# Kernel optimization log

Hardware: AMD Instinct MI355X
Metric: run time of the kernel (lower is better)

Reference implementation:

```python
import jax, jax.numpy as jnp
import numpy as np

FRAME = 1024
ENC = 256
HID = 128
EPS = 1e-7


def _lstm_cell(x, h, c, Wih, Whh, bih, bhh):
    # PyTorch LSTM gate order: i, f, g, o
    z = Wih @ x + bih + Whh @ h + bhh  # [4H]
    i, f, g, o = jnp.split(z, 4)
    i = jax.nn.sigmoid(i)
    f = jax.nn.sigmoid(f)
    g = jnp.tanh(g)
    o = jax.nn.sigmoid(o)
    c_new = f * c + i * g
    h_new = o * jnp.tanh(c_new)
    return h_new, c_new


def setup_inputs() -> dict:
    key = jax.random.key(0)
    ks = jax.random.split(key, 20)
    s = 0.05
    return {
        "y1": jax.random.normal(ks[0], (FRAME,), jnp.float32),
        "h1_in": jax.random.normal(ks[1], (HID,), jnp.float32),
        "c1_in": jax.random.normal(ks[2], (HID,), jnp.float32),
        "h2_in": jax.random.normal(ks[3], (HID,), jnp.float32),
        "c2_in": jax.random.normal(ks[4], (HID,), jnp.float32),
        "enc_W": jax.random.normal(ks[5], (ENC, FRAME), jnp.float32) * s,
        "gamma": jnp.ones((ENC,), jnp.float32),
        "beta": jnp.zeros((ENC,), jnp.float32),
        "Wih1": jax.random.normal(ks[6], (4 * HID, ENC), jnp.float32) * s,
        "Whh1": jax.random.normal(ks[7], (4 * HID, HID), jnp.float32) * s,
        "bih1": jax.random.normal(ks[8], (4 * HID,), jnp.float32) * s,
        "bhh1": jax.random.normal(ks[9], (4 * HID,), jnp.float32) * s,
        "Wih2": jax.random.normal(ks[10], (4 * HID, HID), jnp.float32) * s,
        "Whh2": jax.random.normal(ks[11], (4 * HID, HID), jnp.float32) * s,
        "bih2": jax.random.normal(ks[12], (4 * HID,), jnp.float32) * s,
        "bhh2": jax.random.normal(ks[13], (4 * HID,), jnp.float32) * s,
        "dense_W": jax.random.normal(ks[14], (ENC, HID), jnp.float32) * s,
        "dense_b": jax.random.normal(ks[15], (ENC,), jnp.float32) * s,
        "dec_W": jax.random.normal(ks[16], (FRAME, ENC), jnp.float32) * s,
    }


def reference(y1, h1_in, c1_in, h2_in, c2_in, enc_W, gamma, beta,
              Wih1, Whh1, bih1, bhh1, Wih2, Whh2, bih2, bhh2,
              dense_W, dense_b, dec_W):
    # encoder 1x1 conv == matvec: [256,1024] @ [1024]
    enc = enc_W @ y1  # [256]
    # global-statistic instant layer norm (mean/var over ALL elements)
    mean = jnp.mean(enc)
    sub = enc - mean
    var = jnp.mean(jnp.square(sub))
    enc_norm = (sub / jnp.sqrt(var + EPS)) * gamma + beta
    # two stateful LSTM cells (seq_len=1; dropout is identity at inference)
    h1, c1 = _lstm_cell(enc_norm, h1_in, c1_in, Wih1, Whh1, bih1, bhh1)
    h2, c2 = _lstm_cell(h1, h2_in, c2_in, Wih2, Whh2, bih2, bhh2)
    # dense + sigmoid mask on UN-normalized encoded features
    mask = jax.nn.sigmoid(dense_W @ h2 + dense_b)  # [256]
    estimated = mask * enc
    # decoder 1x1 conv == matvec: [1024,256] @ [256]
    decoded = dec_W @ estimated  # [1024]
    return (decoded.reshape(1, FRAME, 1),
            h1.reshape(1, 1, HID), c1.reshape(1, 1, HID),
            h2.reshape(1, 1, HID), c2.reshape(1, 1, HID))
```

## Files before the change

kernel.cpp:

```cpp
#include <hip/hip_runtime.h>
#include <math.h>


#define FRAME 1024
#define ENC 256
#define HID 128

__device__ __forceinline__ float sigmoidf_(float x) { return 1.0f / (1.0f + __expf(-x)); }
__device__ __forceinline__ float tanhf_(float x) { return 2.0f * sigmoidf_(2.0f * x) - 1.0f; }

__device__ __forceinline__ float wred(float v) {
#pragma unroll
    for (int o = 32; o > 0; o >>= 1) v += __shfl_xor(v, o);
    return v;
}

__global__ __launch_bounds__(256) void k_enc(const float* __restrict__ enc_W,
                                             const float* __restrict__ y1,
                                             float* __restrict__ enc_g) {
    const int t = threadIdx.x, lane = t & 63, w = t >> 6, row = blockIdx.x;
    const float4 a = reinterpret_cast<const float4*>(enc_W + row * FRAME)[t];
    const float4 b = reinterpret_cast<const float4*>(y1)[t];
    float p = a.x * b.x + a.y * b.y + a.z * b.z + a.w * b.w;
    p = wred(p);
    __shared__ float red[4];
    if (lane == 0) red[w] = p;
    __syncthreads();
    if (t == 0) enc_g[row] = red[0] + red[1] + red[2] + red[3];
}

__global__ __launch_bounds__(256) void k_z1(
    const float* __restrict__ enc_g, const float* __restrict__ gamma,
    const float* __restrict__ beta, const float* __restrict__ Wih1,
    const float* __restrict__ Whh1, const float* __restrict__ bih1,
    const float* __restrict__ bhh1, const float* __restrict__ h1_in,
    const float* __restrict__ c1_in, float* __restrict__ h1_g,
    float* __restrict__ out) {
    const int t = threadIdx.x, lane = t & 63, w = t >> 6, b = blockIdx.x;
    __shared__ __align__(16) float encN[ENC];
    __shared__ __align__(16) float hs[HID];
    __shared__ float red[8];
    __shared__ float zsh[4];

    const int r = b + HID * w;
    const float4 wa = reinterpret_cast<const float4*>(Wih1 + r * ENC)[lane];
    const float2 wb = reinterpret_cast<const float2*>(Whh1 + r * HID)[lane];
    const float bias = bih1[r] + bhh1[r];

    const float e = enc_g[t];
    const float s1 = wred(e);
    const float s2 = wred(e * e);
    if (lane == 0) { red[w] = s1; red[4 + w] = s2; }
    if (t < HID) hs[t] = h1_in[t];
    __syncthreads();
    const float mean = (red[0] + red[1] + red[2] + red[3]) * (1.f / ENC);
    const float var  = (red[4] + red[5] + red[6] + red[7]) * (1.f / ENC) - mean * mean;
    const float inv  = rsqrtf(var + 1e-7f);
    encN[t] = (e - mean) * inv * gamma[t] + beta[t];
    __syncthreads();

    const float4 xa = reinterpret_cast<const float4*>(encN)[lane];
    const float2 xb = reinterpret_cast<const float2*>(hs)[lane];
    float p = wa.x * xa.x + wa.y * xa.y + wa.z * xa.z + wa.w * xa.w
            + wb.x * xb.x + wb.y * xb.y;
    p = wred(p);
    if (lane == 0) zsh[w] = p + bias;
    __syncthreads();
    if (t == 0) {
        const float i = sigmoidf_(zsh[0]);
        const float f = sigmoidf_(zsh[1]);
        const float g = tanhf_(zsh[2]);
        const float o = sigmoidf_(zsh[3]);
        const float c = f * c1_in[b] + i * g;
        const float h = o * tanhf_(c);
        h1_g[b] = h;
        out[FRAME + b] = h;
        out[FRAME + HID + b] = c;
    }
}

__global__ __launch_bounds__(256) void k_z2(
    const float* __restrict__ h1_g, const float* __restrict__ h2_in,
    const float* __restrict__ Wih2, const float* __restrict__ Whh2,
    const float* __restrict__ bih2, const float* __restrict__ bhh2,
    const float* __restrict__ c2_in, float* __restrict__ h2_g,
    float* __restrict__ out) {
    const int t = threadIdx.x, lane = t & 63, w = t >> 6, b = blockIdx.x;
    __shared__ __align__(16) float hA[HID];
    __shared__ __align__(16) float hB[HID];
    __shared__ float zsh[4];

    const int r = b + HID * w;
    const float2 wa = reinterpret_cast<const float2*>(Wih2 + r * HID)[lane];
    const float2 wb = reinterpret_cast<const float2*>(Whh2 + r * HID)[lane];
    const float bias = bih2[r] + bhh2[r];

    if (t < HID) { hA[t] = h1_g[t]; hB[t] = h2_in[t]; }
    __syncthreads();
    const float2 xa = reinterpret_cast<const float2*>(hA)[lane];
    const float2 xb = reinterpret_cast<const float2*>(hB)[lane];
    float p = wa.x * xa.x + wa.y * xa.y + wb.x * xb.x + wb.y * xb.y;
    p = wred(p);
    if (lane == 0) zsh[w] = p + bias;
    __syncthreads();
    if (t == 0) {
        const float i = sigmoidf_(zsh[0]);
        const float f = sigmoidf_(zsh[1]);
        const float g = tanhf_(zsh[2]);
        const float o = sigmoidf_(zsh[3]);
        const float c = f * c2_in[b] + i * g;
        const float h = o * tanhf_(c);
        h2_g[b] = h;
        out[FRAME + 2 * HID + b] = h;
        out[FRAME + 3 * HID + b] = c;
    }
}

__global__ __launch_bounds__(256) void k_mask(
    const float* __restrict__ h2_g, const float* __restrict__ dense_W,
    const float* __restrict__ dense_b, const float* __restrict__ enc_g,
    float* __restrict__ est_g) {
    const int t = threadIdx.x, lane = t & 63, w = t >> 6;
    __shared__ __align__(16) float hs[HID];
    const int r = blockIdx.x * 4 + w;
    const float2 wd = reinterpret_cast<const float2*>(dense_W + r * HID)[lane];
    if (t < HID) hs[t] = h2_g[t];
    __syncthreads();
    const float2 xd = reinterpret_cast<const float2*>(hs)[lane];
    float p = wd.x * xd.x + wd.y * xd.y;
    p = wred(p);
    if (lane == 0) est_g[r] = sigmoidf_(p + dense_b[r]) * enc_g[r];
}

__global__ __launch_bounds__(256) void k_dec(
    const float* __restrict__ dec_W, const float* __restrict__ est_g,
    float* __restrict__ out) {
    const int t = threadIdx.x, lane = t & 63, w = t >> 6;
    __shared__ __align__(16) float es[ENC];
    es[t] = est_g[t];
    __syncthreads();
    const int r = blockIdx.x * 4 + w;
    const float4 a = reinterpret_cast<const float4*>(dec_W + r * ENC)[lane];
    const float4 b = reinterpret_cast<const float4*>(es)[lane];
    float p = a.x * b.x + a.y * b.y + a.z * b.z + a.w * b.w;
    p = wred(p);
    if (lane == 0) out[r] = p;
}

extern "C" void kernel_launch(void* const* d_in, const int* in_sizes, int n_in,
                              void* d_out, int out_size, void* d_ws, size_t ws_size,
                              hipStream_t stream) {
    const float* y1      = (const float*)d_in[0];
    const float* h1_in   = (const float*)d_in[1];
    const float* c1_in   = (const float*)d_in[2];
    const float* h2_in   = (const float*)d_in[3];
    const float* c2_in   = (const float*)d_in[4];
    const float* enc_W   = (const float*)d_in[5];
    const float* gamma   = (const float*)d_in[6];
    const float* beta    = (const float*)d_in[7];
    const float* Wih1    = (const float*)d_in[8];
    const float* Whh1    = (const float*)d_in[9];
    const float* bih1    = (const float*)d_in[10];
    const float* bhh1    = (const float*)d_in[11];
    const float* Wih2    = (const float*)d_in[12];
    const float* Whh2    = (const float*)d_in[13];
    const float* bih2    = (const float*)d_in[14];
    const float* bhh2    = (const float*)d_in[15];
    const float* dense_W = (const float*)d_in[16];
    const float* dense_b = (const float*)d_in[17];
    const float* dec_W   = (const float*)d_in[18];

    float* out   = (float*)d_out;
    float* ws    = (float*)d_ws;
    float* enc_g = ws;
    float* h1_g  = ws + 256;
    float* h2_g  = ws + 384;
    float* est_g = ws + 512;

    k_enc <<<256, 256, 0, stream>>>(enc_W, y1, enc_g);
    k_z1  <<<128, 256, 0, stream>>>(enc_g, gamma, beta, Wih1, Whh1, bih1, bhh1,
                                    h1_in, c1_in, h1_g, out);
    k_z2  <<<128, 256, 0, stream>>>(h1_g, h2_in, Wih2, Whh2, bih2, bhh2,
                                    c2_in, h2_g, out);
    k_mask<<<64, 256, 0, stream>>>(h2_g, dense_W, dense_b, enc_g, est_g);
    k_dec <<<256, 256, 0, stream>>>(dec_W, est_g, out);
}
```

Before: 19.08 us.

## Hoist recurrent matvecs into encoder launch and fuse LSTM2, mask, decoder kernels

The Whh·h recurrent products plus biases for both LSTM cells are computed in extra blocks of the encoder kernel, since they do not depend on the encoder output. LSTM2, the dense mask and the decoder are merged into a single kernel in which every block redundantly recomputes the 128x512 Wih2 matvec and the 256x128 dense matvec, then does its own slice of the decoder. This cuts the launch count from five to three. The cost is redundant weight reads from cache and more serial work per block.

Result: slower. 27.54 us (+44.3%).

```diff
diff --git a/kernel.cpp b/kernel.cpp
--- a/kernel.cpp
+++ b/kernel.cpp
@@ -15,43 +15,66 @@
     return v;
 }
 
-__global__ __launch_bounds__(256) void k_enc(const float* __restrict__ enc_W,
-                                             const float* __restrict__ y1,
-                                             float* __restrict__ enc_g) {
-    const int t = threadIdx.x, lane = t & 63, w = t >> 6, row = blockIdx.x;
-    const float4 a = reinterpret_cast<const float4*>(enc_W + row * FRAME)[t];
-    const float4 b = reinterpret_cast<const float4*>(y1)[t];
-    float p = a.x * b.x + a.y * b.y + a.z * b.z + a.w * b.w;
-    p = wred(p);
-    __shared__ float red[4];
-    if (lane == 0) red[w] = p;
-    __syncthreads();
-    if (t == 0) enc_g[row] = red[0] + red[1] + red[2] + red[3];
+__global__ __launch_bounds__(256) void k_enc(
+    const float* __restrict__ enc_W, const float* __restrict__ y1,
+    const float* __restrict__ Whh1, const float* __restrict__ bih1,
+    const float* __restrict__ bhh1, const float* __restrict__ h1_in,
+    const float* __restrict__ Whh2, const float* __restrict__ bih2,
+    const float* __restrict__ bhh2, const float* __restrict__ h2_in,
+    float* __restrict__ enc_g, float* __restrict__ ph1, float* __restrict__ ph2) {
+    const int t = threadIdx.x, lane = t & 63, w = t >> 6, bid = blockIdx.x;
+    if (bid < 256) {
+        const float4 a = reinterpret_cast<const float4*>(enc_W + bid * FRAME)[t];
+        const float4 b = reinterpret_cast<const float4*>(y1)[t];
+        float p = a.x * b.x + a.y * b.y + a.z * b.z + a.w * b.w;
+        p = wred(p);
+        __shared__ float red[4];
+        if (lane == 0) red[w] = p;
+        __syncthreads();
+        if (t == 0) enc_g[bid] = red[0] + red[1] + red[2] + red[3];
+    } else if (bid < 320) {
+        const int pb = bid - 256;
+#pragma unroll
+        for (int j = 0; j < 2; ++j) {
+            const int r = pb * 8 + w * 2 + j;
+            const float2 a = reinterpret_cast<const float2*>(Whh1 + r * HID)[lane];
+            const float2 b = reinterpret_cast<const float2*>(h1_in)[lane];
+            float p = a.x * b.x + a.y * b.y;
+            p = wred(p);
+            if (lane == 0) ph1[r] = p + bih1[r] + bhh1[r];
+        }
+    } else {
+        const int pb = bid - 320;
+#pragma unroll
+        for (int j = 0; j < 2; ++j) {
+            const int r = pb * 8 + w * 2 + j;
+            const float2 a = reinterpret_cast<const float2*>(Whh2 + r * HID)[lane];
+            const float2 b = reinterpret_cast<const float2*>(h2_in)[lane];
+            float p = a.x * b.x + a.y * b.y;
+            p = wred(p);
+            if (lane == 0) ph2[r] = p + bih2[r] + bhh2[r];
+        }
+    }
 }
 
 __global__ __launch_bounds__(256) void k_z1(
     const float* __restrict__ enc_g, const float* __restrict__ gamma,
     const float* __restrict__ beta, const float* __restrict__ Wih1,
-    const float* __restrict__ Whh1, const float* __restrict__ bih1,
-    const float* __restrict__ bhh1, const float* __restrict__ h1_in,
-    const float* __restrict__ c1_in, float* __restrict__ h1_g,
-    float* __restrict__ out) {
+    const float* __restrict__ ph1, const float* __restrict__ c1_in,
+    float* __restrict__ h1_g, float* __restrict__ out) {
     const int t = threadIdx.x, lane = t & 63, w = t >> 6, b = blockIdx.x;
     __shared__ __align__(16) float encN[ENC];
-    __shared__ __align__(16) float hs[HID];
     __shared__ float red[8];
     __shared__ float zsh[4];
 
     const int r = b + HID * w;
     const float4 wa = reinterpret_cast<const float4*>(Wih1 + r * ENC)[lane];
-    const float2 wb = reinterpret_cast<const float2*>(Whh1 + r * HID)[lane];
-    const float bias = bih1[r] + bhh1[r];
+    const float ph = ph1[r];
 
     const float e = enc_g[t];
     const float s1 = wred(e);
     const float s2 = wred(e * e);
     if (lane == 0) { red[w] = s1; red[4 + w] = s2; }
-    if (t < HID) hs[t] = h1_in[t];
     __syncthreads();
     const float mean = (red[0] + red[1] + red[2] + red[3]) * (1.f / ENC);
     const float var  = (red[4] + red[5] + red[6] + red[7]) * (1.f / ENC) - mean * mean;
@@ -60,11 +83,9 @@
     __syncthreads();
 
     const float4 xa = reinterpret_cast<const float4*>(encN)[lane];
-    const float2 xb = reinterpret_cast<const float2*>(hs)[lane];
-    float p = wa.x * xa.x + wa.y * xa.y + wa.z * xa.z + wa.w * xa.w
-            + wb.x * xb.x + wb.y * xb.y;
+    float p = wa.x * xa.x + wa.y * xa.y + wa.z * xa.z + wa.w * xa.w;
     p = wred(p);
-    if (lane == 0) zsh[w] = p + bias;
+    if (lane == 0) zsh[w] = p + ph;
     __syncthreads();
     if (t == 0) {
         const float i = sigmoidf_(zsh[0]);
@@ -79,72 +100,94 @@
     }
 }
 
-__global__ __launch_bounds__(256) void k_z2(
-    const float* __restrict__ h1_g, const float* __restrict__ h2_in,
-    const float* __restrict__ Wih2, const float* __restrict__ Whh2,
-    const float* __restrict__ bih2, const float* __restrict__ bhh2,
-    const float* __restrict__ c2_in, float* __restrict__ h2_g,
+__global__ __launch_bounds__(256) void k_rest(
+    const float* __restrict__ h1_g, const float* __restrict__ Wih2,
+    const float* __restrict__ ph2, const float* __restrict__ c2_in,
+    const float* __restrict__ dense_W, const float* __restrict__ dense_b,
+    const float* __restrict__ enc_g, const float* __restrict__ dec_W,
     float* __restrict__ out) {
-    const int t = threadIdx.x, lane = t & 63, w = t >> 6, b = blockIdx.x;
-    __shared__ __align__(16) float hA[HID];
-    __shared__ __align__(16) float hB[HID];
-    __shared__ float zsh[4];
-
-    const int r = b + HID * w;
-    const float2 wa = reinterpret_cast<const float2*>(Wih2 + r * HID)[lane];
-    const float2 wb = reinterpret_cast<const float2*>(Whh2 + r * HID)[lane];
-    const float bias = bih2[r] + bhh2[r];
-
-    if (t < HID) { hA[t] = h1_g[t]; hB[t] = h2_in[t]; }
-    __syncthreads();
-    const float2 xa = reinterpret_cast<const float2*>(hA)[lane];
-    const float2 xb = reinterpret_cast<const float2*>(hB)[lane];
-    float p = wa.x * xa.x + wa.y * xa.y + wb.x * xb.x + wb.y * xb.y;
-    p = wred(p);
-    if (lane == 0) zsh[w] = p + bias;
-    __syncthreads();
-    if (t == 0) {
-        const float i = sigmoidf_(zsh[0]);
-        const float f = sigmoidf_(zsh[1]);
-        const float g = tanhf_(zsh[2]);
-        const float o = sigmoidf_(zsh[3]);
-        const float c = f * c2_in[b] + i * g;
+    const int t = threadIdx.x, lane = t & 63, w = t >> 6, bid = blockIdx.x;
+    const int sub = lane >> 2, q = lane & 3;
+
+    __shared__ __align__(16) float h1s[HID];
+    __shared__ __align__(16) float h2s[HID];
+    __shared__ __align__(16) float zz[4 * HID];
+    __shared__ __align__(16) float encL[ENC];
+    __shared__ __align__(16) float es[ENC];
+
+    if (t < HID) h1s[t] = h1_g[t];
+    if (t < ENC) encL[t] = enc_g[t];
+    __syncthreads();
+
+    {
+        const float4* x4 = reinterpret_cast<const float4*>(h1s);
+        float4 xv[8];
+#pragma unroll
+        for (int j = 0; j < 8; ++j) xv[j] = x4[q * 8 + j];
+#pragma unroll
+        for (int p = 0; p < 8; ++p) {
+            const int r = w * 128 + p * 16 + sub;
+            const float4* W4 = reinterpret_cast<const float4*>(Wih2 + r * HID);
+            float4 acc = {0.f, 0.f, 0.f, 0.f};
+#pragma unroll
+            for (int j = 0; j < 8; ++j) {
+                const float4 a = W4[q * 8 + j];
+                acc.x += a.x * xv[j].x; acc.y += a.y * xv[j].y;
+                acc.z += a.z * xv[j].z; acc.w += a.w * xv[j].w;
+            }
+            float s = acc.x + acc.y + acc.z + acc.w;
+            s += __shfl_xor(s, 1); s += __shfl_xor(s, 2);
+            if (q == 0) zz[r] = s + ph2[r];
+        }
+    }
+    __syncthreads();
+
+    if (t < HID) {
+        const float i = sigmoidf_(zz[t]);
+        const float f = sigmoidf_(zz[HID + t]);
+        const float g = tanhf_(zz[2 * HID + t]);
+        const float o = sigmoidf_(zz[3 * HID + t]);
+        const float c = f * c2_in[t] + i * g;
         const float h = o * tanhf_(c);
-        h2_g[b] = h;
-        out[FRAME + 2 * HID + b] = h;
-        out[FRAME + 3 * HID + b] = c;
-    }
-}
-
-__global__ __launch_bounds__(256) void k_mask(
-    const float* __restrict__ h2_g, const float* __restrict__ dense_W,
-    const float* __restrict__ dense_b, const float* __restrict__ enc_g,
-    float* __restrict__ est_g) {
-    const int t = threadIdx.x, lane = t & 63, w = t >> 6;
-    __shared__ __align__(16) float hs[HID];
-    const int r = blockIdx.x * 4 + w;
-    const float2 wd = reinterpret_cast<const float2*>(dense_W + r * HID)[lane];
-    if (t < HID) hs[t] = h2_g[t];
-    __syncthreads();
-    const float2 xd = reinterpret_cast<const float2*>(hs)[lane];
-    float p = wd.x * xd.x + wd.y * xd.y;
-    p = wred(p);
-    if (lane == 0) est_g[r] = sigmoidf_(p + dense_b[r]) * enc_g[r];
-}
-
-__global__ __launch_bounds__(256) void k_dec(
-    const float* __restrict__ dec_W, const float* __restrict__ est_g,
-    float* __restrict__ out) {
-    const int t = threadIdx.x, lane = t & 63, w = t >> 6;
-    __shared__ __align__(16) float es[ENC];
-    es[t] = est_g[t];
-    __syncthreads();
-    const int r = blockIdx.x * 4 + w;
-    const float4 a = reinterpret_cast<const float4*>(dec_W + r * ENC)[lane];
-    const float4 b = reinterpret_cast<const float4*>(es)[lane];
-    float p = a.x * b.x + a.y * b.y + a.z * b.z + a.w * b.w;
-    p = wred(p);
-    if (lane == 0) out[r] = p;
+        h2s[t] = h;
+        if (bid == 0) { out[FRAME + 2 * HID + t] = h; out[FRAME + 3 * HID + t] = c; }
+    }
+    __syncthreads();
+
+    {
+        const float4* x4 = reinterpret_cast<const float4*>(h2s);
+        float4 xv[8];
+#pragma unroll
+        for (int j = 0; j < 8; ++j) xv[j] = x4[q * 8 + j];
+#pragma unroll
+        for (int p = 0; p < 4; ++p) {
+            const int r = w * 64 + p * 16 + sub;
+            const float4* W4 = reinterpret_cast<const float4*>(dense_W + r * HID);
+            float4 acc = {0.f, 0.f, 0.f, 0.f};
+#pragma unroll
+            for (int j = 0; j < 8; ++j) {
+                const float4 a = W4[q * 8 + j];
+                acc.x += a.x * xv[j].x; acc.y += a.y * xv[j].y;
+                acc.z += a.z * xv[j].z; acc.w += a.w * xv[j].w;
+            }
+            float s = acc.x + acc.y + acc.z + acc.w;
+            s += __shfl_xor(s, 1); s += __shfl_xor(s, 2);
+            if (q == 0) es[r] = sigmoidf_(s + dense_b[r]) * encL[r];
+        }
+    }
+    __syncthreads();
+
+    {
+        const float4 xe = reinterpret_cast<const float4*>(es)[lane];
+#pragma unroll
+        for (int j = 0; j < 2; ++j) {
+            const int r = bid * 8 + w * 2 + j;
+            const float4 a = reinterpret_cast<const float4*>(dec_W + r * ENC)[lane];
+            float s = a.x * xe.x + a.y * xe.y + a.z * xe.z + a.w * xe.w;
+            s = wred(s);
+            if (lane == 0) out[r] = s;
+        }
+    }
 }
 
 extern "C" void kernel_launch(void* const* d_in, const int* in_sizes, int n_in,
@@ -173,15 +216,13 @@
     float* out   = (float*)d_out;
     float* ws    = (float*)d_ws;
     float* enc_g = ws;
-    float* h1_g  = ws + 256;
-    float* h2_g  = ws + 384;
-    float* est_g = ws + 512;
-
-    k_enc <<<256, 256, 0, stream>>>(enc_W, y1, enc_g);
-    k_z1  <<<128, 256, 0, stream>>>(enc_g, gamma, beta, Wih1, Whh1, bih1, bhh1,
-                                    h1_in, c1_in, h1_g, out);
-    k_z2  <<<128, 256, 0, stream>>>(h1_g, h2_in, Wih2, Whh2, bih2, bhh2,
-                                    c2_in, h2_g, out);
-    k_mask<<<64, 256, 0, stream>>>(h2_g, dense_W, dense_b, enc_g, est_g);
-    k_dec <<<256, 256, 0, stream>>>(dec_W, est_g, out);
-}
+    float* ph1   = ws + 256;
+    float* ph2   = ws + 768;
+    float* h1_g  = ws + 1280;
+
+    k_enc <<<384, 256, 0, stream>>>(enc_W, y1, Whh1, bih1, bhh1, h1_in,
+                                    Whh2, bih2, bhh2, h2_in, enc_g, ph1, ph2);
+    k_z1  <<<128, 256, 0, stream>>>(enc_g, gamma, beta, Wih1, ph1, c1_in, h1_g, out);
+    k_rest<<<128, 256, 0, stream>>>(h1_g, Wih2, ph2, c2_in, dense_W, dense_b,
+                                    enc_g, dec_W, out);
+}
```

## Fuse dense mask matvec into LSTM2 kernel via padded atomic accumulation

Applied to the files above, without the earlier changes.

Removes the separate k_mask launch. Each LSTM2 block now multiplies its h2 element by one column of dense_W and atomically adds the product into an accumulator padded to avoid false sharing, which k_z1 zeroes beforehand. The sigmoid and the multiply by enc move into the prologue of k_dec. This saves one kernel launch and its dependency gap, at the cost of 32K float atomics and uncoalesced column reads of dense_W.

Result: no change. 19.44 us (+1.9%).

```diff
diff --git a/kernel.cpp b/kernel.cpp
--- a/kernel.cpp
+++ b/kernel.cpp
@@ -5,6 +5,7 @@
 #define FRAME 1024
 #define ENC 256
 #define HID 128
+#define MSTRIDE 32
 
 __device__ __forceinline__ float sigmoidf_(float x) { return 1.0f / (1.0f + __expf(-x)); }
 __device__ __forceinline__ float tanhf_(float x) { return 2.0f * sigmoidf_(2.0f * x) - 1.0f; }
@@ -35,7 +36,7 @@
     const float* __restrict__ Whh1, const float* __restrict__ bih1,
     const float* __restrict__ bhh1, const float* __restrict__ h1_in,
     const float* __restrict__ c1_in, float* __restrict__ h1_g,
-    float* __restrict__ out) {
+    float* __restrict__ macc, float* __restrict__ out) {
     const int t = threadIdx.x, lane = t & 63, w = t >> 6, b = blockIdx.x;
     __shared__ __align__(16) float encN[ENC];
     __shared__ __align__(16) float hs[HID];
@@ -46,6 +47,8 @@
     const float4 wa = reinterpret_cast<const float4*>(Wih1 + r * ENC)[lane];
     const float2 wb = reinterpret_cast<const float2*>(Whh1 + r * HID)[lane];
     const float bias = bih1[r] + bhh1[r];
+
+    if (b < 32 && t < 8) macc[(b * 8 + t) * MSTRIDE] = 0.0f;
 
     const float e = enc_g[t];
     const float s1 = wred(e);
@@ -83,17 +86,19 @@
     const float* __restrict__ h1_g, const float* __restrict__ h2_in,
     const float* __restrict__ Wih2, const float* __restrict__ Whh2,
     const float* __restrict__ bih2, const float* __restrict__ bhh2,
-    const float* __restrict__ c2_in, float* __restrict__ h2_g,
-    float* __restrict__ out) {
+    const float* __restrict__ c2_in, const float* __restrict__ dense_W,
+    float* __restrict__ macc, float* __restrict__ out) {
     const int t = threadIdx.x, lane = t & 63, w = t >> 6, b = blockIdx.x;
     __shared__ __align__(16) float hA[HID];
     __shared__ __align__(16) float hB[HID];
     __shared__ float zsh[4];
+    __shared__ float h2sh;
 
     const int r = b + HID * w;
     const float2 wa = reinterpret_cast<const float2*>(Wih2 + r * HID)[lane];
     const float2 wb = reinterpret_cast<const float2*>(Whh2 + r * HID)[lane];
     const float bias = bih2[r] + bhh2[r];
+    const float dcol = dense_W[t * HID + b];
 
     if (t < HID) { hA[t] = h1_g[t]; hB[t] = h2_in[t]; }
     __syncthreads();
@@ -110,39 +115,27 @@
         const float o = sigmoidf_(zsh[3]);
         const float c = f * c2_in[b] + i * g;
         const float h = o * tanhf_(c);
-        h2_g[b] = h;
+        h2sh = h;
         out[FRAME + 2 * HID + b] = h;
         out[FRAME + 3 * HID + b] = c;
     }
-}
-
-__global__ __launch_bounds__(256) void k_mask(
-    const float* __restrict__ h2_g, const float* __restrict__ dense_W,
-    const float* __restrict__ dense_b, const float* __restrict__ enc_g,
-    float* __restrict__ est_g) {
-    const int t = threadIdx.x, lane = t & 63, w = t >> 6;
-    __shared__ __align__(16) float hs[HID];
-    const int r = blockIdx.x * 4 + w;
-    const float2 wd = reinterpret_cast<const float2*>(dense_W + r * HID)[lane];
-    if (t < HID) hs[t] = h2_g[t];
     __syncthreads();
-    const float2 xd = reinterpret_cast<const float2*>(hs)[lane];
-    float p = wd.x * xd.x + wd.y * xd.y;
-    p = wred(p);
-    if (lane == 0) est_g[r] = sigmoidf_(p + dense_b[r]) * enc_g[r];
+    atomicAdd(&macc[t * MSTRIDE], dcol * h2sh);
 }
 
 __global__ __launch_bounds__(256) void k_dec(
-    const float* __restrict__ dec_W, const float* __restrict__ est_g,
+    const float* __restrict__ dec_W, const float* __restrict__ macc,
+    const float* __restrict__ dense_b, const float* __restrict__ enc_g,
     float* __restrict__ out) {
     const int t = threadIdx.x, lane = t & 63, w = t >> 6;
     __shared__ __align__(16) float es[ENC];
-    es[t] = est_g[t];
+    const float m = macc[t * MSTRIDE];
+    es[t] = sigmoidf_(m + dense_b[t]) * enc_g[t];
     __syncthreads();
     const int r = blockIdx.x * 4 + w;
     const float4 a = reinterpret_cast<const float4*>(dec_W + r * ENC)[lane];
-    const float4 b = reinterpret_cast<const float4*>(es)[lane];
-    float p = a.x * b.x + a.y * b.y + a.z * b.z + a.w * b.w;
+    const float4 bb = reinterpret_cast<const float4*>(es)[lane];
+    float p = a.x * bb.x + a.y * bb.y + a.z * bb.z + a.w * bb.w;
     p = wred(p);
     if (lane == 0) out[r] = p;
 }
@@ -174,14 +167,12 @@
     float* ws    = (float*)d_ws;
     float* enc_g = ws;
     float* h1_g  = ws + 256;
-    float* h2_g  = ws + 384;
-    float* est_g = ws + 512;
+    float* macc  = ws + 512;
 
-    k_enc <<<256, 256, 0, stream>>>(enc_W, y1, enc_g);
-    k_z1  <<<128, 256, 0, stream>>>(enc_g, gamma, beta, Wih1, Whh1, bih1, bhh1,
-                                    h1_in, c1_in, h1_g, out);
-    k_z2  <<<128, 256, 0, stream>>>(h1_g, h2_in, Wih2, Whh2, bih2, bhh2,
-                                    c2_in, h2_g, out);
-    k_mask<<<64, 256, 0, stream>>>(h2_g, dense_W, dense_b, enc_g, est_g);
-    k_dec <<<256, 256, 0, stream>>>(dec_W, est_g, out);
+    k_enc<<<256, 256, 0, stream>>>(enc_W, y1, enc_g);
+    k_z1 <<<128, 256, 0, stream>>>(enc_g, gamma, beta, Wih1, Whh1, bih1, bhh1,
+                                   h1_in, c1_in, h1_g, macc, out);
+    k_z2 <<<128, 256, 0, stream>>>(h1_g, h2_in, Wih2, Whh2, bih2, bhh2,
+                                   c2_in, dense_W, macc, out);
+    k_dec<<<256, 256, 0, stream>>>(dec_W, macc, dense_b, enc_g, out);
 }
```
